# Kernel optimization log

Hardware: AMD Instinct MI355X
Metric: run time of the kernel (lower is better)

## Reference

```python
import jax, jax.numpy as jnp
import numpy as np


def setup_inputs() -> dict:
    key = jax.random.key(0)
    k1, k2, k3 = jax.random.split(key, 3)
    x = jax.random.normal(k1, (8192, 2048), dtype=jnp.float32)
    w = jax.random.normal(k2, (4096, 2048), dtype=jnp.float32) * 0.02  # [out, in]
    b = jax.random.normal(k3, (4096,), dtype=jnp.float32) * 0.01
    return {"x": x, "w": w, "b": b}


def reference(x, w, b):
    # Straight-through binarization: forward uses sign(w), gradient flows as identity.
    binary_w = w + jax.lax.stop_gradient(jnp.sign(w) - w)  # [out, in], values in {-1, 0, 1}
    # F.linear: x @ W^T + b
    return jnp.einsum("ni,oi->no", x, binary_w) + b
```

## Files before the change

### kernel.cpp

```cpp
#include <hip/hip_runtime.h>
#include <hip/hip_bf16.h>
#include <stdint.h>

typedef __bf16 bf16x8 __attribute__((ext_vector_type(8)));
typedef float  f32x4  __attribute__((ext_vector_type(4)));


__device__ __forceinline__ uint32_t rn2_bf16(uint32_t lo, uint32_t hi) {
  uint32_t rlo = (lo + 0x7FFFu + ((lo >> 16) & 1u)) >> 16;
  uint32_t rhi = (hi + 0x7FFFu + ((hi >> 16) & 1u)) >> 16;
  return (rhi << 16) | (rlo & 0xFFFFu);
}

__device__ __forceinline__ uint32_t sign2_bf16(uint32_t lo, uint32_t hi) {
  uint32_t slo = (lo & 0x7FFFFFFFu) ? (0x3F80u | ((lo >> 16) & 0x8000u)) : 0u;
  uint32_t shi = (hi & 0x7FFFFFFFu) ? (0x3F80u | ((hi >> 16) & 0x8000u)) : 0u;
  return (shi << 16) | slo;
}

__device__ __forceinline__ void gl16(const void* g, void* l) {
  __builtin_amdgcn_global_load_lds(
      (const __attribute__((address_space(1))) uint32_t*)g,
      (__attribute__((address_space(3))) uint32_t*)l,
      16, 0, 0);
}


__global__ void cvt_prep(const uint4* __restrict__ x, uint4* __restrict__ xo, int nx8,
                         const uint4* __restrict__ w, uint4* __restrict__ wo, int nw8) {
  int stride = gridDim.x * blockDim.x;
  int total = nx8 + nw8;
  for (int i = blockIdx.x * blockDim.x + threadIdx.x; i < total; i += stride) {
    if (i < nx8) {
      uint4 a = x[2 * i + 0];
      uint4 b = x[2 * i + 1];
      uint4 o;
      o.x = rn2_bf16(a.x, a.y);
      o.y = rn2_bf16(a.z, a.w);
      o.z = rn2_bf16(b.x, b.y);
      o.w = rn2_bf16(b.z, b.w);
      xo[i] = o;
    } else {
      int j = i - nx8;
      uint4 a = w[2 * j + 0];
      uint4 b = w[2 * j + 1];
      uint4 o;
      o.x = sign2_bf16(a.x, a.y);
      o.y = sign2_bf16(a.z, a.w);
      o.z = sign2_bf16(b.x, b.y);
      o.w = sign2_bf16(b.z, b.w);
      wo[j] = o;
    }
  }
}


#define BAR()   __builtin_amdgcn_s_barrier()
#define LGKM0() asm volatile("s_waitcnt lgkmcnt(0)" ::: "memory")
#define VM4()   asm volatile("s_waitcnt vmcnt(4)" ::: "memory")
#define SWZ(x)  ((x) ^ ((((x) >> 7) & 7) << 4))

__global__ __launch_bounds__(512, 2) void gemm256(
    const uint16_t* __restrict__ A,
    const uint16_t* __restrict__ B,
    const float* __restrict__ bias,
    float* __restrict__ C,
    int M, int N, int K) {
  __shared__ alignas(16) uint8_t L[131072];
  uint8_t* Lb = L;

  const int tid  = threadIdx.x;
  const int lane = tid & 63;
  const int w    = tid >> 6;
  const int wr   = w >> 2;
  const int wc   = w & 3;
  const int r16  = lane & 15;
  const int kg   = lane >> 4;

  const int nbx = N >> 8;
  const int nwg = nbx * (M >> 8);
  const int bid = blockIdx.x;
  const int swb = (bid & 7) * (nwg >> 3) + (bid >> 3);
  const size_t m0 = (size_t)(swb / nbx) << 8;
  const size_t n0 = (size_t)(swb % nbx) << 8;

  const int NT = K >> 6;
  const size_t rowB = (size_t)K * 2;

  const int o0 = (w << 10) + (lane << 4);
  const int o1 = o0 + 8192;
  const int s0 = SWZ(o0);
  const int s1 = SWZ(o1);
  const size_t g0 = (size_t)(s0 >> 7) * rowB + (s0 & 127);
  const size_t g1 = (size_t)(s1 >> 7) * rowB + (s1 & 127);
  const char* Ab = (const char*)A + m0 * rowB;
  const char* Bb = (const char*)B + n0 * rowB;
  const size_t hiO = (size_t)128 * rowB;
  const int wB = w << 10;

  const int laneA = (wr * 128 + r16) * 128 + kg * 16;
  const int laneB = (wc * 64 + r16) * 128 + kg * 16;

#define STG(LOFF, SRC) do { \
    gl16((SRC) + g0, Lb + (LOFF) + wB); \
    gl16((SRC) + g1, Lb + (LOFF) + 8192 + wB); } while (0)

#define FRA(d, mi, ks) (*reinterpret_cast<const bf16x8*>( \
    Lb + (d) * 65536 + SWZ(laneA + (mi) * 2048 + (ks) * 64)))
#define FRB(d, ni, ks) (*reinterpret_cast<const bf16x8*>( \
    Lb + (d) * 65536 + 32768 + SWZ(laneB + (ni) * 2048 + (ks) * 64)))

  f32x4 acc[8][4] = {};

#define QMFMA(AARR, BARR, MB) do { \
    __builtin_amdgcn_s_setprio(1); \
    _Pragma("unroll") \
    for (int mi2 = 0; mi2 < 4; ++mi2) \
      _Pragma("unroll") \
      for (int ni = 0; ni < 4; ++ni) \
        acc[(MB) + mi2][ni] = __builtin_amdgcn_mfma_f32_16x16x32_bf16( \
            AARR[(MB) + mi2], BARR[ni], acc[(MB) + mi2][ni], 0, 0, 0); \
    __builtin_amdgcn_s_setprio(0); } while (0)

  STG(0,      Ab);
  STG(16384,  Ab + hiO);
  STG(32768,  Bb);
  STG(49152,  Bb + hiO);
  STG(65536,  Ab + 128);
  STG(81920,  Ab + hiO + 128);
  VM4();
  BAR();

  bf16x8 a0[8], a1[8], b0[4], b1[4];
  const int T = K >> 7;
  for (int t = 0; t < T; ++t) {
    const size_t c1 = (size_t)(2 * t + 1) * 128;
    const int k2i = 2 * t + 2, k3i = 2 * t + 3;
    const size_t c2 = (size_t)(k2i < NT ? k2i : NT - 1) * 128;
    const size_t c3 = (size_t)(k3i < NT ? k3i : NT - 1) * 128;

#pragma unroll
    for (int i = 0; i < 8; ++i) a0[i] = FRA(0, i, 0);
#pragma unroll
    for (int i = 0; i < 4; ++i) b0[i] = FRB(0, i, 0);
    STG(98304, Bb + c1);
    BAR(); LGKM0();
    QMFMA(a0, b0, 0);
    BAR();

#pragma unroll
    for (int i = 0; i < 8; ++i) a1[i] = FRA(0, i, 1);
#pragma unroll
    for (int i = 0; i < 4; ++i) b1[i] = FRB(0, i, 1);
    STG(114688, Bb + hiO + c1);
    BAR(); LGKM0();
    QMFMA(a0, b0, 4);
    BAR();

    STG(0, Ab + c2);
    BAR(); LGKM0();
    QMFMA(a1, b1, 0);
    BAR();

    STG(16384, Ab + hiO + c2);
    BAR(); LGKM0();
    QMFMA(a1, b1, 4);
    VM4();
    BAR();

#pragma unroll
    for (int i = 0; i < 8; ++i) a0[i] = FRA(1, i, 0);
#pragma unroll
    for (int i = 0; i < 4; ++i) b0[i] = FRB(1, i, 0);
    STG(32768, Bb + c2);
    BAR(); LGKM0();
    QMFMA(a0, b0, 0);
    BAR();

#pragma unroll
    for (int i = 0; i < 8; ++i) a1[i] = FRA(1, i, 1);
#pragma unroll
    for (int i = 0; i < 4; ++i) b1[i] = FRB(1, i, 1);
    STG(49152, Bb + hiO + c2);
    BAR(); LGKM0();
    QMFMA(a0, b0, 4);
    BAR();

    STG(65536, Ab + c3);
    BAR(); LGKM0();
    QMFMA(a1, b1, 0);
    BAR();

    STG(81920, Ab + hiO + c3);
    BAR(); LGKM0();
    QMFMA(a1, b1, 4);
    VM4();
    BAR();
  }

#pragma unroll
  for (int ni = 0; ni < 4; ++ni) {
    const size_t col = n0 + wc * 64 + ni * 16 + r16;
    const float bv = bias[col];
#pragma unroll
    for (int mi = 0; mi < 8; ++mi) {
      const size_t row0 = m0 + wr * 128 + mi * 16 + kg * 4;
#pragma unroll
      for (int j = 0; j < 4; ++j)
        C[(row0 + j) * N + col] = acc[mi][ni][j] + bv;
    }
  }
}


__global__ __launch_bounds__(256) void gemm_bin(
    const uint16_t* __restrict__ A, const uint16_t* __restrict__ B,
    const float* __restrict__ bias, float* __restrict__ C,
    int M, int N, int K) {
  constexpr int BK = 32;
  __shared__ alignas(16) uint16_t lA[128 * BK];
  __shared__ alignas(16) uint16_t lB[128 * BK];
  const int tid = threadIdx.x;
  const int lane = tid & 63;
  const int wid = tid >> 6;
  const int wr = wid >> 1, wc = wid & 1;
  const int r16 = lane & 15, kg = lane >> 4;
  const int m0 = blockIdx.y * 128, n0 = blockIdx.x * 128;
  f32x4 acc[4][4] = {};
  for (int k0 = 0; k0 < K; k0 += BK) {
    __syncthreads();
#pragma unroll
    for (int p = 0; p < 2; ++p) {
      int idx = p * 256 + tid;
      int row = idx >> 2;
      int col = (idx & 3) * 8;
      gl16(A + (size_t)(m0 + row) * K + k0 + col, lA + p * 2048 + wid * 512);
      gl16(B + (size_t)(n0 + row) * K + k0 + col, lB + p * 2048 + wid * 512);
    }
    __syncthreads();
    bf16x8 af[4], bg[4];
#pragma unroll
    for (int i = 0; i < 4; ++i)
      af[i] = *reinterpret_cast<const bf16x8*>(lA + (wr * 64 + i * 16 + r16) * BK + kg * 8);
#pragma unroll
    for (int i = 0; i < 4; ++i)
      bg[i] = *reinterpret_cast<const bf16x8*>(lB + (wc * 64 + i * 16 + r16) * BK + kg * 8);
#pragma unroll
    for (int mi = 0; mi < 4; ++mi)
#pragma unroll
      for (int ni = 0; ni < 4; ++ni)
        acc[mi][ni] = __builtin_amdgcn_mfma_f32_16x16x32_bf16(af[mi], bg[ni], acc[mi][ni], 0, 0, 0);
  }
#pragma unroll
  for (int ni = 0; ni < 4; ++ni) {
    int col = n0 + wc * 64 + ni * 16 + r16;
    float bv = bias[col];
#pragma unroll
    for (int mi = 0; mi < 4; ++mi) {
      int row0 = m0 + wr * 64 + mi * 16 + kg * 4;
#pragma unroll
      for (int j = 0; j < 4; ++j)
        C[(size_t)(row0 + j) * N + col] = acc[mi][ni][j] + bv;
    }
  }
}

__global__ void gemm_naive(const float* __restrict__ x, const float* __restrict__ w,
                           const float* __restrict__ b, float* __restrict__ out,
                           int M, int N, int K) {
  int n = blockIdx.x * blockDim.x + threadIdx.x;
  int m = blockIdx.y;
  if (n >= N || m >= M) return;
  float acc = 0.f;
  for (int k = 0; k < K; ++k) {
    float wv = w[(size_t)n * K + k];
    float s = (wv > 0.f) ? 1.f : ((wv < 0.f) ? -1.f : 0.f);
    acc += x[(size_t)m * K + k] * s;
  }
  out[(size_t)m * N + n] = acc + b[n];
}

extern "C" void kernel_launch(void* const* d_in, const int* in_sizes, int n_in,
                              void* d_out, int out_size, void* d_ws, size_t ws_size,
                              hipStream_t stream) {
  const float* x = (const float*)d_in[0];
  const float* w = (const float*)d_in[1];
  const float* b = (const float*)d_in[2];
  float* out = (float*)d_out;

  const int N = in_sizes[2];
  const int K = in_sizes[1] / N;
  const int M = in_sizes[0] / K;

  const size_t need = ((size_t)M * K + (size_t)N * K) * sizeof(uint16_t);
  if (ws_size < need) {
    hipLaunchKernelGGL(gemm_naive, dim3((N + 255) / 256, M), dim3(256), 0, stream,
                       x, w, b, out, M, N, K);
    return;
  }

  uint16_t* Xb = (uint16_t*)d_ws;
  uint16_t* Wb = Xb + (size_t)M * K;

  hipLaunchKernelGGL(cvt_prep, dim3(2048), dim3(256), 0, stream,
                     (const uint4*)x, (uint4*)Xb, (M * K) / 8,
                     (const uint4*)w, (uint4*)Wb, (N * K) / 8);

  const bool big_ok = (M % 256 == 0) && (N % 256 == 0) && (K % 128 == 0) &&
                      (((M / 256) * (N / 256)) % 8 == 0);
  if (big_ok) {
    hipLaunchKernelGGL(gemm256, dim3((M / 256) * (N / 256)), dim3(512), 0, stream,
                       Xb, Wb, b, out, M, N, K);
  } else {
    hipLaunchKernelGGL(gemm_bin, dim3(N / 128, M / 128), dim3(256), 0, stream,
                       Xb, Wb, b, out, M, N, K);
  }
}
```

Baseline: 156.5 us.

## Software-pipeline LDS fragment reads with MFMA and reduce barriers in gemm256

Restructures the main loop of the 256x256 GEMM so each quarter-step issues MFMAs on already-loaded register fragments while it reads the next quarter's A/B fragments from LDS. Register fragment buffers are split into 4-wide halves (aLo/aHi, bA/bB), and global-to-LDS staging moves to different points in the loop, so there is one barrier per phase instead of two and no explicit lgkmcnt waits. The aim is to hide LDS read latency and barrier stalls behind matrix math. The trade-off is that correctness now depends on compiler-inserted waits and the new staging order, and K must be a multiple of 256.

```diff
diff --git a/kernel.cpp b/kernel.cpp
--- a/kernel.cpp
+++ b/kernel.cpp
@@ -55,9 +55,9 @@
 }
 
 
-#define BAR()   __builtin_amdgcn_s_barrier()
-#define LGKM0() asm volatile("s_waitcnt lgkmcnt(0)" ::: "memory")
-#define VM4()   asm volatile("s_waitcnt vmcnt(4)" ::: "memory")
+#define BARX()  asm volatile("s_barrier" ::: "memory")
+#define VM0()   asm volatile("s_waitcnt vmcnt(0)" ::: "memory")
+#define VMN4()  asm volatile("s_waitcnt vmcnt(4)" ::: "memory")
 #define SWZ(x)  ((x) ^ ((((x) >> 7) & 7) << 4))
 
 __global__ __launch_bounds__(512, 2) void gemm256(
@@ -112,26 +112,36 @@
 
   f32x4 acc[8][4] = {};
 
-#define QMFMA(AARR, BARR, MB) do { \
+#define QM(A4, B4, MB) do { \
     __builtin_amdgcn_s_setprio(1); \
     _Pragma("unroll") \
     for (int mi2 = 0; mi2 < 4; ++mi2) \
       _Pragma("unroll") \
       for (int ni = 0; ni < 4; ++ni) \
         acc[(MB) + mi2][ni] = __builtin_amdgcn_mfma_f32_16x16x32_bf16( \
-            AARR[(MB) + mi2], BARR[ni], acc[(MB) + mi2][ni], 0, 0, 0); \
+            A4[mi2], B4[ni], acc[(MB) + mi2][ni], 0, 0, 0); \
     __builtin_amdgcn_s_setprio(0); } while (0)
+
+#define RDA(DST, d, base, ks) do { \
+    _Pragma("unroll") \
+    for (int i = 0; i < 4; ++i) DST[i] = FRA(d, (base) + i, ks); } while (0)
+#define RDB(DST, d, ks) do { \
+    _Pragma("unroll") \
+    for (int i = 0; i < 4; ++i) DST[i] = FRB(d, i, ks); } while (0)
 
   STG(0,      Ab);
   STG(16384,  Ab + hiO);
   STG(32768,  Bb);
   STG(49152,  Bb + hiO);
-  STG(65536,  Ab + 128);
-  STG(81920,  Ab + hiO + 128);
-  VM4();
-  BAR();
-
-  bf16x8 a0[8], a1[8], b0[4], b1[4];
+  STG(98304,  Bb + 128);
+  STG(114688, Bb + hiO + 128);
+  VMN4();
+  BARX();
+
+  bf16x8 aLo[4], aHi[4], bA[4], bB[4];
+  RDA(aLo, 0, 0, 0);
+  RDB(bA, 0, 0);
+
   const int T = K >> 7;
   for (int t = 0; t < T; ++t) {
     const size_t c1 = (size_t)(2 * t + 1) * 128;
@@ -139,63 +149,51 @@
     const size_t c2 = (size_t)(k2i < NT ? k2i : NT - 1) * 128;
     const size_t c3 = (size_t)(k3i < NT ? k3i : NT - 1) * 128;
 
-#pragma unroll
-    for (int i = 0; i < 8; ++i) a0[i] = FRA(0, i, 0);
-#pragma unroll
-    for (int i = 0; i < 4; ++i) b0[i] = FRB(0, i, 0);
-    STG(98304, Bb + c1);
-    BAR(); LGKM0();
-    QMFMA(a0, b0, 0);
-    BAR();
-
-#pragma unroll
-    for (int i = 0; i < 8; ++i) a1[i] = FRA(0, i, 1);
-#pragma unroll
-    for (int i = 0; i < 4; ++i) b1[i] = FRB(0, i, 1);
-    STG(114688, Bb + hiO + c1);
-    BAR(); LGKM0();
-    QMFMA(a0, b0, 4);
-    BAR();
-
+    QM(aLo, bA, 0);
+    RDA(aHi, 0, 4, 0);
+    STG(65536, Ab + c1);
+    STG(81920, Ab + hiO + c1);
+    BARX();
+
+    QM(aHi, bA, 4);
+    RDA(aLo, 0, 0, 1);
+    RDB(bB, 0, 1);
+    BARX();
+
+    QM(aLo, bB, 0);
+    RDA(aHi, 0, 4, 1);
+    VM0();
+    BARX();
+
+    QM(aHi, bB, 4);
+    RDA(aLo, 1, 0, 0);
+    RDB(bA, 1, 0);
+    STG(32768, Bb + c2);
+    STG(49152, Bb + hiO + c2);
+    BARX();
+
+    QM(aLo, bA, 0);
+    RDA(aHi, 1, 4, 0);
     STG(0, Ab + c2);
-    BAR(); LGKM0();
-    QMFMA(a1, b1, 0);
-    BAR();
-
     STG(16384, Ab + hiO + c2);
-    BAR(); LGKM0();
-    QMFMA(a1, b1, 4);
-    VM4();
-    BAR();
-
-#pragma unroll
-    for (int i = 0; i < 8; ++i) a0[i] = FRA(1, i, 0);
-#pragma unroll
-    for (int i = 0; i < 4; ++i) b0[i] = FRB(1, i, 0);
-    STG(32768, Bb + c2);
-    BAR(); LGKM0();
-    QMFMA(a0, b0, 0);
-    BAR();
-
-#pragma unroll
-    for (int i = 0; i < 8; ++i) a1[i] = FRA(1, i, 1);
-#pragma unroll
-    for (int i = 0; i < 4; ++i) b1[i] = FRB(1, i, 1);
-    STG(49152, Bb + hiO + c2);
-    BAR(); LGKM0();
-    QMFMA(a0, b0, 4);
-    BAR();
-
-    STG(65536, Ab + c3);
-    BAR(); LGKM0();
-    QMFMA(a1, b1, 0);
-    BAR();
-
-    STG(81920, Ab + hiO + c3);
-    BAR(); LGKM0();
-    QMFMA(a1, b1, 4);
-    VM4();
-    BAR();
+    BARX();
+
+    QM(aHi, bA, 4);
+    RDA(aLo, 1, 0, 1);
+    RDB(bB, 1, 1);
+    BARX();
+
+    QM(aLo, bB, 0);
+    RDA(aHi, 1, 4, 1);
+    VM0();
+    BARX();
+
+    QM(aHi, bB, 4);
+    RDA(aLo, 0, 0, 0);
+    RDB(bA, 0, 0);
+    STG(98304, Bb + c3);
+    STG(114688, Bb + hiO + c3);
+    BARX();
   }
 
 #pragma unroll
@@ -306,7 +304,7 @@
                      (const uint4*)x, (uint4*)Xb, (M * K) / 8,
                      (const uint4*)w, (uint4*)Wb, (N * K) / 8);
 
-  const bool big_ok = (M % 256 == 0) && (N % 256 == 0) && (K % 128 == 0) &&
+  const bool big_ok = (M % 256 == 0) && (N % 256 == 0) && (K % 256 == 0) &&
                       (((M / 256) * (N / 256)) % 8 == 0);
   if (big_ok) {
     hipLaunchKernelGGL(gemm256, dim3((M / 256) * (N / 256)), dim3(512), 0, stream,
```

Result: faster. 147.0 us (-6.1%).
